# Optimization experiments

Hardware: AMD Instinct MI355X
Metric: run time of the kernel (lower is better)

## Reference

```python
import jax, jax.numpy as jnp
import numpy as np


def conv3x3(x, w, b):
    # stride 1, pad 1, NCHW / OIHW
    out = jax.lax.conv_general_dilated(x, w, (1, 1), ((1, 1), (1, 1)),
                                       dimension_numbers=('NCHW', 'OIHW', 'NCHW'))
    return out + b[None, :, None, None]


def bilinear_sample(x, ys, xs):
    # x: [B,C,H,W]; ys,xs: [B,K,H,W] float sampling coords.
    # mmcv-style: zero outside image, per-corner validity.
    B, C, H, W = x.shape
    x_flat = x.reshape(B, C, H * W)
    y0 = jnp.floor(ys)
    x0 = jnp.floor(xs)
    dy = ys - y0
    dx = xs - x0
    y0i = y0.astype(jnp.int32)
    x0i = x0.astype(jnp.int32)

    def corner(yc, xc, wgt):
        valid = (yc >= 0) & (yc < H) & (xc >= 0) & (xc < W)
        idx = jnp.clip(yc, 0, H - 1) * W + jnp.clip(xc, 0, W - 1)  # [B,K,H,W]
        idx_f = idx.reshape(B, -1)
        vals = jax.vmap(lambda xf, ix: xf[:, ix])(x_flat, idx_f)  # [B,C,K*H*W]
        vals = vals.reshape(B, C, *yc.shape[1:])
        return vals * (wgt * valid)[:, None]

    out = corner(y0i, x0i, (1 - dy) * (1 - dx))
    out = out + corner(y0i, x0i + 1, (1 - dy) * dx)
    out = out + corner(y0i + 1, x0i, dy * (1 - dx))
    out = out + corner(y0i + 1, x0i + 1, dy * dx)
    return out  # [B,C,K,H,W]


def avgpool3s2(z):
    # AvgPool2d(kernel=3, stride=2, padding=1), count_include_pad=True -> divide by 9
    s = jax.lax.reduce_window(z, 0.0, jax.lax.add, (1, 1, 3, 3), (1, 1, 2, 2),
                              ((0, 0), (0, 0), (1, 1), (1, 1)))
    return s / 9.0


def setup_inputs() -> dict:
    key = jax.random.key(0)
    k1, k2, k3 = jax.random.split(key, 3)
    C = 64
    x = jax.random.normal(k1, (4, C, 128, 128), dtype=jnp.float32)
    w_off = jax.random.normal(k2, (27, C, 3, 3), dtype=jnp.float32) * 0.02
    b_off = jnp.zeros((27,), dtype=jnp.float32)
    w_align = jax.random.normal(k3, (C, C, 3, 3), dtype=jnp.float32) * 0.02
    b_align = jnp.zeros((C,), dtype=jnp.float32)
    return {"x": x, "w_off": w_off, "b_off": b_off, "w_align": w_align, "b_align": b_align}


def reference(x, w_off, b_off, w_align, b_align):
    B, C, H, W = x.shape
    K = 9
    off_all = conv3x3(x, w_off, b_off)               # [B,27,H,W]
    offset = off_all[:, :2 * K]                      # [B,18,H,W]
    mask = 2.0 * jax.nn.sigmoid(off_all[:, 2 * K:])  # [B,9,H,W]
    off = offset.reshape(B, K, 2, H, W)
    dy = off[:, :, 0]
    dx = off[:, :, 1]
    # base kernel grid (dilation 1, pad 1): offsets in {-1,0,1}
    ky = (jnp.arange(K) // 3 - 1).astype(jnp.float32)
    kx = (jnp.arange(K) % 3 - 1).astype(jnp.float32)
    ys = jnp.arange(H, dtype=jnp.float32)[None, None, :, None] + ky[None, :, None, None] + dy
    xs = jnp.arange(W, dtype=jnp.float32)[None, None, None, :] + kx[None, :, None, None] + dx
    sampled = bilinear_sample(x, ys, xs) * mask[:, None]    # [B,C,K,H,W]
    w = jnp.einsum('bckhw,ock->bohw', sampled, w_align.reshape(C, C, K))
    w = w + b_align[None, :, None, None]
    w = jnp.exp(jax.nn.sigmoid(w))
    return avgpool3s2(w * x) / avgpool3s2(w)
```

## Files before the change

kernel.cpp:

```cpp
#include <hip/hip_runtime.h>
#include <hip/hip_bf16.h>

#define HW 16384
#define CC 64
#define BB 4

typedef __attribute__((ext_vector_type(8))) short bf8;
typedef __attribute__((ext_vector_type(4))) float f4;

static __device__ __forceinline__ unsigned short f2bf(float f) {
    __hip_bfloat16 h = __float2bfloat16(f);
    return *reinterpret_cast<unsigned short*>(&h);
}
static __device__ __forceinline__ float lo16f(unsigned u) { return __uint_as_float(u << 16); }
static __device__ __forceinline__ float hi16f(unsigned u) { return __uint_as_float(u & 0xFFFF0000u); }
static __device__ __forceinline__ unsigned rne_pack(float flo, float fhi) {
    unsigned a = __float_as_uint(flo);
    unsigned b = __float_as_uint(fhi);
    a += 0x7FFFu + ((a >> 16) & 1u);
    b += 0x7FFFu + ((b >> 16) & 1u);
    return __builtin_amdgcn_perm(b, a, 0x07060302u);
}

__global__ __launch_bounds__(256) void k_prep_tx(const float* __restrict__ x,
                                                 const float* __restrict__ w_off,
                                                 const float* __restrict__ w_align,
                                                 unsigned short* __restrict__ xT,
                                                 unsigned short* __restrict__ wA2,
                                                 unsigned short* __restrict__ Wal2) {
    __shared__ unsigned T32[64 * 33];
    int bx = blockIdx.x, t = threadIdx.x;
    if (bx < 216) {
        int i = bx * 256 + t;
        if (i < 32 * 576) {
            int jj = i & 7;
            int chunk = i >> 3;
            int l = chunk & 63;
            int g = chunk >> 6;
            int m2 = g & 1;
            int h2 = (g >> 1) & 1;
            int tp = g >> 2;
            int m = m2 * 16 + (l & 15);
            int c = h2 * 32 + (l >> 4) * 8 + jj;
            float v = (m < 27) ? w_off[m * 576 + c * 9 + tp] : 0.f;
            wA2[i] = f2bf(v);
        } else {
            int j = i - 32 * 576;
            int jj = j & 7;
            int chunk = j >> 3;
            int l = chunk & 63;
            int g = chunk >> 6;
            int mt = g & 3;
            int th = g >> 2;
            int h2 = th & 1;
            int tp = th >> 1;
            int o = mt * 16 + (l & 15);
            int c = h2 * 32 + (l >> 4) * 8 + jj;
            Wal2[j] = f2bf(w_align[o * 576 + c * 9 + tp]);
        }
        return;
    }
    int pix0 = (bx - 216) * 64;
    int b = pix0 >> 14, hw0 = pix0 & (HW - 1);
    const float* xb = x + (size_t)b * CC * HW + hw0;
#pragma unroll
    for (int u = 0; u < 8; u++) {
        int i = t + 256 * u;
        int cp = i >> 6, p = i & 63;
        float v0 = xb[(size_t)(2 * cp) * HW + p];
        float v1 = xb[(size_t)(2 * cp + 1) * HW + p];
        T32[p * 33 + cp] = (unsigned)f2bf(v0) | ((unsigned)f2bf(v1) << 16);
    }
    __syncthreads();
#pragma unroll
    for (int u = 0; u < 2; u++) {
        int i = t + 256 * u;
        int p = i >> 3, q = i & 7;
        uint4 qq;
        qq.x = T32[p * 33 + q * 4 + 0];
        qq.y = T32[p * 33 + q * 4 + 1];
        qq.z = T32[p * 33 + q * 4 + 2];
        qq.w = T32[p * 33 + q * 4 + 3];
        *(uint4*)(xT + ((size_t)b * HW + hw0 + p) * CC + q * 8) = qq;
    }
}

#define MIXD(P,M) rne_pack( \
    P##w0*lo16f(P##q0.M)+P##w1*lo16f(P##q1.M)+P##w2*lo16f(P##q2.M)+P##w3*lo16f(P##q3.M), \
    P##w0*hi16f(P##q0.M)+P##w1*hi16f(P##q1.M)+P##w2*hi16f(P##q2.M)+P##w3*hi16f(P##q3.M))
#define MIXD2(P,M) rne_pack( \
    P##w0*lo16f(P##q4.M)+P##w1*lo16f(P##q5.M)+P##w2*lo16f(P##q6.M)+P##w3*lo16f(P##q7.M), \
    P##w0*hi16f(P##q4.M)+P##w1*hi16f(P##q5.M)+P##w2*hi16f(P##q6.M)+P##w3*hi16f(P##q7.M))

#define PREP(j,P) { \
    float dy_ = OB[(2*(j))*133+pxo]; \
    float dx_ = OB[(2*(j)+1)*133+pxo]; \
    float m_  = OB[(18+(j))*133+pxo]; \
    const int k3_ = (j)/3, kx_ = (j)-3*k3_; \
    float ys_ = (float)(hp+k3_-1)+dy_, xs_ = (float)(wp+kx_-1)+dx_; \
    float y0f_ = floorf(ys_), x0f_ = floorf(xs_); \
    float fy_ = ys_-y0f_, fx_ = xs_-x0f_; \
    int y0_ = (int)y0f_, x0_ = (int)x0f_, y1_ = y0_+1, x1_ = x0_+1; \
    bool vy0_ = (unsigned)y0_<128u, vy1_ = (unsigned)y1_<128u; \
    bool vx0_ = (unsigned)x0_<128u, vx1_ = (unsigned)x1_<128u; \
    int cy0_ = min(max(y0_,0),127), cy1_ = min(max(y1_,0),127); \
    int cx0_ = min(max(x0_,0),127), cx1_ = min(max(x1_,0),127); \
    P##w0 = (1.f-fy_)*(1.f-fx_)*((vy0_&&vx0_)?m_:0.f); \
    P##w1 = (1.f-fy_)*fx_      *((vy0_&&vx1_)?m_:0.f); \
    P##w2 = fy_*(1.f-fx_)      *((vy1_&&vx0_)?m_:0.f); \
    P##w3 = fy_*fx_            *((vy1_&&vx1_)?m_:0.f); \
    bool inT_ = (cy0_>=hm2)&(cy1_<=hp3)&(cx0_>=wm3)&(cx1_<=wp66); \
    int r0_ = (cy0_-hm2)*70-wm3, r1_ = (cy1_-hm2)*70-wm3; \
    int e00_ = r0_+cx0_, e01_ = r0_+cx1_, e10_ = r1_+cx0_, e11_ = r1_+cx1_; \
    const unsigned short* p00_ = inT_ ? (TFg + e00_*64 + ((quad^(e00_&7))<<3)) \
        : xTb + ((size_t)((cy0_<<7)+cx0_))*CC + quad*8; \
    const unsigned short* p01_ = inT_ ? (TFg + e01_*64 + ((quad^(e01_&7))<<3)) \
        : xTb + ((size_t)((cy0_<<7)+cx1_))*CC + quad*8; \
    const unsigned short* p10_ = inT_ ? (TFg + e10_*64 + ((quad^(e10_&7))<<3)) \
        : xTb + ((size_t)((cy1_<<7)+cx0_))*CC + quad*8; \
    const unsigned short* p11_ = inT_ ? (TFg + e11_*64 + ((quad^(e11_&7))<<3)) \
        : xTb + ((size_t)((cy1_<<7)+cx1_))*CC + quad*8; \
    P##q0 = *(const uint4*)p00_; \
    P##q1 = *(const uint4*)p01_; \
    P##q2 = *(const uint4*)p10_; \
    P##q3 = *(const uint4*)p11_; \
    P##q4 = *(const uint4*)((unsigned long long)p00_ ^ 64ull); \
    P##q5 = *(const uint4*)((unsigned long long)p01_ ^ 64ull); \
    P##q6 = *(const uint4*)((unsigned long long)p10_ ^ 64ull); \
    P##q7 = *(const uint4*)((unsigned long long)p11_ ^ 64ull); \
}

#define TAP(j,P) { \
    uint4 f0_; \
    f0_.x = MIXD(P,x); f0_.y = MIXD(P,y); f0_.z = MIXD(P,z); f0_.w = MIXD(P,w); \
    uint4 f1_; \
    f1_.x = MIXD2(P,x); f1_.y = MIXD2(P,y); f1_.z = MIXD2(P,z); f1_.w = MIXD2(P,w); \
    bf8 bf0_ = *(const bf8*)&f0_; \
    bf8 bf1_ = *(const bf8*)&f1_; \
    const bf8 a0_ = *(const bf8*)(wl + (size_t)((((j)*2+0)*4+0)*512)); \
    const bf8 a1_ = *(const bf8*)(wl + (size_t)((((j)*2+0)*4+1)*512)); \
    const bf8 a2_ = *(const bf8*)(wl + (size_t)((((j)*2+0)*4+2)*512)); \
    const bf8 a3_ = *(const bf8*)(wl + (size_t)((((j)*2+0)*4+3)*512)); \
    acc[0] = __builtin_amdgcn_mfma_f32_16x16x32_bf16(a0_, bf0_, acc[0], 0, 0, 0); \
    acc[1] = __builtin_amdgcn_mfma_f32_16x16x32_bf16(a1_, bf0_, acc[1], 0, 0, 0); \
    acc[2] = __builtin_amdgcn_mfma_f32_16x16x32_bf16(a2_, bf0_, acc[2], 0, 0, 0); \
    acc[3] = __builtin_amdgcn_mfma_f32_16x16x32_bf16(a3_, bf0_, acc[3], 0, 0, 0); \
    const bf8 a4_ = *(const bf8*)(wl + (size_t)((((j)*2+1)*4+0)*512)); \
    const bf8 a5_ = *(const bf8*)(wl + (size_t)((((j)*2+1)*4+1)*512)); \
    const bf8 a6_ = *(const bf8*)(wl + (size_t)((((j)*2+1)*4+2)*512)); \
    const bf8 a7_ = *(const bf8*)(wl + (size_t)((((j)*2+1)*4+3)*512)); \
    acc[0] = __builtin_amdgcn_mfma_f32_16x16x32_bf16(a4_, bf1_, acc[0], 0, 0, 0); \
    acc[1] = __builtin_amdgcn_mfma_f32_16x16x32_bf16(a5_, bf1_, acc[1], 0, 0, 0); \
    acc[2] = __builtin_amdgcn_mfma_f32_16x16x32_bf16(a6_, bf1_, acc[2], 0, 0, 0); \
    acc[3] = __builtin_amdgcn_mfma_f32_16x16x32_bf16(a7_, bf1_, acc[3], 0, 0, 0); \
}

__global__ __launch_bounds__(512, 3) void k_fused(const unsigned short* __restrict__ xT,
                                                  const unsigned short* __restrict__ wA2,
                                                  const unsigned short* __restrict__ Wal2,
                                                  const float* __restrict__ b_off,
                                                  const float* __restrict__ b_align,
                                                  float* __restrict__ wten) {
    __shared__ __align__(16) unsigned short TF[420 * 64];
    __shared__ float OB[27 * 133];

    int t = threadIdx.x, lane = t & 63, wv = t >> 6;
    int quad = lane >> 4, col = lane & 15;
    int bx = blockIdx.x;
    int b = bx >> 7;
    int r = bx & 127;
    int h0 = (r >> 1) * 2;
    int w0 = (r & 1) * 64;
    int pxo = wv * 16 + col;
    int rr = pxo >> 6;
    int hp = h0 + rr, wp = w0 + (pxo & 63);
    int px = (hp << 7) + wp;
    const unsigned short* xTb = xT + (size_t)b * HW * CC;
    const unsigned short* wl = Wal2 + lane * 8;
    const unsigned short* TFg = TF;

#pragma unroll
    for (int u = 0; u < 7; u++) {
        int i = t + 512 * u;
        if (i < 3360) {
            int e = i >> 3, s = i & 7;
            int ty = e / 70, tx = e - ty * 70;
            int gy = min(max(h0 - 2 + ty, 0), 127);
            int gx = min(max(w0 - 3 + tx, 0), 127);
            int c = s ^ (e & 7);
            uint4 q = *(const uint4*)(xTb + ((size_t)((gy << 7) + gx)) * CC + c * 8);
            *(uint4*)(TF + i * 8) = q;
        }
    }
    __syncthreads();

    {
        const bf8 zero = {0, 0, 0, 0, 0, 0, 0, 0};
        f4 a0 = {0.f, 0.f, 0.f, 0.f};
        f4 a1 = {0.f, 0.f, 0.f, 0.f};
#pragma unroll
        for (int tap = 0; tap < 9; tap++) {
            int dyt = tap / 3 - 1, dxt = tap - (tap / 3) * 3 - 1;
            int hs = hp + dyt, ws = wp + dxt;
            bool valid = ((unsigned)hs < 128u) && ((unsigned)ws < 128u);
            int e = (rr + dyt + 2) * 70 + (pxo & 63) + dxt + 3;
            int sL = quad ^ (e & 7);
            bf8 b0 = *(const bf8*)(TF + e * 64 + (sL << 3));
            bf8 b1 = *(const bf8*)(TF + e * 64 + ((sL ^ 4) << 3));
            b0 = valid ? b0 : zero;
            b1 = valid ? b1 : zero;
            const bf8 a00 = *(const bf8*)(wA2 + (((tap * 4 + 0) * 64 + lane) << 3));
            const bf8 a01 = *(const bf8*)(wA2 + (((tap * 4 + 1) * 64 + lane) << 3));
            const bf8 a10 = *(const bf8*)(wA2 + (((tap * 4 + 2) * 64 + lane) << 3));
            const bf8 a11 = *(const bf8*)(wA2 + (((tap * 4 + 3) * 64 + lane) << 3));
            a0 = __builtin_amdgcn_mfma_f32_16x16x32_bf16(a00, b0, a0, 0, 0, 0);
            a1 = __builtin_amdgcn_mfma_f32_16x16x32_bf16(a01, b0, a1, 0, 0, 0);
            a0 = __builtin_amdgcn_mfma_f32_16x16x32_bf16(a10, b1, a0, 0, 0, 0);
            a1 = __builtin_amdgcn_mfma_f32_16x16x32_bf16(a11, b1, a1, 0, 0, 0);
        }
#pragma unroll
        for (int i = 0; i < 4; i++) {
            int o0 = quad * 4 + i;
            OB[o0 * 133 + pxo] = a0[i] + b_off[o0];
            int o1 = 16 + o0;
            if (o1 < 27) {
                float v = a1[i] + b_off[o1];
                if (o1 >= 18) v = 2.f / (1.f + __expf(-v));
                OB[o1 * 133 + pxo] = v;
            }
        }
    }

    int hm2 = h0 - 2, hp3 = h0 + 3, wm3 = w0 - 3, wp66 = w0 + 66;

    f4 acc[4];
#pragma unroll
    for (int mt = 0; mt < 4; mt++) acc[mt] = (f4){0.f, 0.f, 0.f, 0.f};

    uint4 Aq0, Aq1, Aq2, Aq3, Aq4, Aq5, Aq6, Aq7;
    uint4 Bq0, Bq1, Bq2, Bq3, Bq4, Bq5, Bq6, Bq7;
    float Aw0, Aw1, Aw2, Aw3, Bw0, Bw1, Bw2, Bw3;

    PREP(0, A);
    PREP(1, B); TAP(0, A);
    PREP(2, A); TAP(1, B);
    PREP(3, B); TAP(2, A);
    PREP(4, A); TAP(3, B);
    PREP(5, B); TAP(4, A);
    PREP(6, A); TAP(5, B);
    PREP(7, B); TAP(6, A);
    PREP(8, A); TAP(7, B);
    TAP(8, A);

    float* wb = wten + (size_t)b * CC * HW + px;
#pragma unroll
    for (int mt = 0; mt < 4; mt++)
#pragma unroll
        for (int i = 0; i < 4; i++) {
            int o = mt * 16 + quad * 4 + i;
            float u = acc[mt][i] + b_align[o];
            float sg = 1.f / (1.f + __expf(-u));
            wb[(size_t)o * HW] = __expf(sg);
        }
}

__global__ __launch_bounds__(256) void k_pool(const float* __restrict__ x,
                                              const float* __restrict__ wten,
                                              float* __restrict__ out) {
    int idx = blockIdx.x * 256 + threadIdx.x;
    int ow = idx & 63;
    int oh = (idx >> 6) & 63;
    int bc = idx >> 12;
    const float* wp = wten + (size_t)bc * HW;
    const float* xp = x + (size_t)bc * HW;
    float num = 0.f, den = 0.f;
#pragma unroll
    for (int iy = 0; iy < 3; iy++) {
        int y = 2 * oh + iy - 1;
        if ((unsigned)y >= 128u) continue;
#pragma unroll
        for (int ix = 0; ix < 3; ix++) {
            int xc = 2 * ow + ix - 1;
            if ((unsigned)xc >= 128u) continue;
            float wv = wp[y * 128 + xc];
            float xv = xp[y * 128 + xc];
            num = fmaf(wv, xv, num);
            den += wv;
        }
    }
    out[idx] = num / den;
}

extern "C" void kernel_launch(void* const* d_in, const int* in_sizes, int n_in,
                              void* d_out, int out_size, void* d_ws, size_t ws_size,
                              hipStream_t stream) {
    const float* x       = (const float*)d_in[0];
    const float* w_off   = (const float*)d_in[1];
    const float* b_off   = (const float*)d_in[2];
    const float* w_align = (const float*)d_in[3];
    const float* b_align = (const float*)d_in[4];
    float* out = (float*)d_out;

    char* p = (char*)d_ws;
    float* wten = (float*)p;                  p += (size_t)BB * CC * HW * 4;
    unsigned short* xT  = (unsigned short*)p; p += (size_t)BB * HW * CC * 2;
    unsigned short* wA2 = (unsigned short*)p; p += 32 * 576 * 2;
    unsigned short* Wal2 = (unsigned short*)p;

    k_prep_tx<<<dim3(1240), dim3(256), 0, stream>>>(x, w_off, w_align, xT, wA2, Wal2);
    k_fused<<<dim3(512), dim3(512), 0, stream>>>(xT, wA2, Wal2, b_off, b_align, wten);
    k_pool<<<dim3(4096), dim3(256), 0, stream>>>(x, wten, out);
}
```

Before: 117.3 us.

## Apply bilinear weights after MFMA instead of mixing corner samples before

Instead of blending the four bilinear corner samples in fp32 and repacking them to bf16 before each MFMA, each corner's raw bf16 values are multiplied by the weights through MFMA separately. The corner weights are then applied to the per-corner results with FMAs into the accumulator. This removes the unpack, mix and RNE-repack ALU work but issues four times as many MFMAs per tap. Launch bounds also go from 3 to 4 blocks per CU, which tightens the register budget.

```diff
diff --git a/kernel.cpp b/kernel.cpp
--- a/kernel.cpp
+++ b/kernel.cpp
@@ -11,15 +11,6 @@
 static __device__ __forceinline__ unsigned short f2bf(float f) {
     __hip_bfloat16 h = __float2bfloat16(f);
     return *reinterpret_cast<unsigned short*>(&h);
-}
-static __device__ __forceinline__ float lo16f(unsigned u) { return __uint_as_float(u << 16); }
-static __device__ __forceinline__ float hi16f(unsigned u) { return __uint_as_float(u & 0xFFFF0000u); }
-static __device__ __forceinline__ unsigned rne_pack(float flo, float fhi) {
-    unsigned a = __float_as_uint(flo);
-    unsigned b = __float_as_uint(fhi);
-    a += 0x7FFFu + ((a >> 16) & 1u);
-    b += 0x7FFFu + ((b >> 16) & 1u);
-    return __builtin_amdgcn_perm(b, a, 0x07060302u);
 }
 
 __global__ __launch_bounds__(256) void k_prep_tx(const float* __restrict__ x,
@@ -84,13 +75,6 @@
         *(uint4*)(xT + ((size_t)b * HW + hw0 + p) * CC + q * 8) = qq;
     }
 }
-
-#define MIXD(P,M) rne_pack( \
-    P##w0*lo16f(P##q0.M)+P##w1*lo16f(P##q1.M)+P##w2*lo16f(P##q2.M)+P##w3*lo16f(P##q3.M), \
-    P##w0*hi16f(P##q0.M)+P##w1*hi16f(P##q1.M)+P##w2*hi16f(P##q2.M)+P##w3*hi16f(P##q3.M))
-#define MIXD2(P,M) rne_pack( \
-    P##w0*lo16f(P##q4.M)+P##w1*lo16f(P##q5.M)+P##w2*lo16f(P##q6.M)+P##w3*lo16f(P##q7.M), \
-    P##w0*hi16f(P##q4.M)+P##w1*hi16f(P##q5.M)+P##w2*hi16f(P##q6.M)+P##w3*hi16f(P##q7.M))
 
 #define PREP(j,P) { \
     float dy_ = OB[(2*(j))*133+pxo]; \
@@ -130,32 +114,31 @@
     P##q7 = *(const uint4*)((unsigned long long)p11_ ^ 64ull); \
 }
 
-#define TAP(j,P) { \
-    uint4 f0_; \
-    f0_.x = MIXD(P,x); f0_.y = MIXD(P,y); f0_.z = MIXD(P,z); f0_.w = MIXD(P,w); \
-    uint4 f1_; \
-    f1_.x = MIXD2(P,x); f1_.y = MIXD2(P,y); f1_.z = MIXD2(P,z); f1_.w = MIXD2(P,w); \
-    bf8 bf0_ = *(const bf8*)&f0_; \
-    bf8 bf1_ = *(const bf8*)&f1_; \
-    const bf8 a0_ = *(const bf8*)(wl + (size_t)((((j)*2+0)*4+0)*512)); \
-    const bf8 a1_ = *(const bf8*)(wl + (size_t)((((j)*2+0)*4+1)*512)); \
-    const bf8 a2_ = *(const bf8*)(wl + (size_t)((((j)*2+0)*4+2)*512)); \
-    const bf8 a3_ = *(const bf8*)(wl + (size_t)((((j)*2+0)*4+3)*512)); \
-    acc[0] = __builtin_amdgcn_mfma_f32_16x16x32_bf16(a0_, bf0_, acc[0], 0, 0, 0); \
-    acc[1] = __builtin_amdgcn_mfma_f32_16x16x32_bf16(a1_, bf0_, acc[1], 0, 0, 0); \
-    acc[2] = __builtin_amdgcn_mfma_f32_16x16x32_bf16(a2_, bf0_, acc[2], 0, 0, 0); \
-    acc[3] = __builtin_amdgcn_mfma_f32_16x16x32_bf16(a3_, bf0_, acc[3], 0, 0, 0); \
-    const bf8 a4_ = *(const bf8*)(wl + (size_t)((((j)*2+1)*4+0)*512)); \
-    const bf8 a5_ = *(const bf8*)(wl + (size_t)((((j)*2+1)*4+1)*512)); \
-    const bf8 a6_ = *(const bf8*)(wl + (size_t)((((j)*2+1)*4+2)*512)); \
-    const bf8 a7_ = *(const bf8*)(wl + (size_t)((((j)*2+1)*4+3)*512)); \
-    acc[0] = __builtin_amdgcn_mfma_f32_16x16x32_bf16(a4_, bf1_, acc[0], 0, 0, 0); \
-    acc[1] = __builtin_amdgcn_mfma_f32_16x16x32_bf16(a5_, bf1_, acc[1], 0, 0, 0); \
-    acc[2] = __builtin_amdgcn_mfma_f32_16x16x32_bf16(a6_, bf1_, acc[2], 0, 0, 0); \
-    acc[3] = __builtin_amdgcn_mfma_f32_16x16x32_bf16(a7_, bf1_, acc[3], 0, 0, 0); \
-}
-
-__global__ __launch_bounds__(512, 3) void k_fused(const unsigned short* __restrict__ xT,
+#define TAP1(j,P,MT) { \
+    const bf8 ah0_ = *(const bf8*)(wl + (size_t)((((j)*2+0)*4+(MT))*512)); \
+    const bf8 ah1_ = *(const bf8*)(wl + (size_t)((((j)*2+1)*4+(MT))*512)); \
+    const f4 z_ = {0.f, 0.f, 0.f, 0.f}; \
+    f4 t0_ = __builtin_amdgcn_mfma_f32_16x16x32_bf16(ah0_, *(const bf8*)&P##q0, z_, 0, 0, 0); \
+    t0_    = __builtin_amdgcn_mfma_f32_16x16x32_bf16(ah1_, *(const bf8*)&P##q4, t0_, 0, 0, 0); \
+    f4 t1_ = __builtin_amdgcn_mfma_f32_16x16x32_bf16(ah0_, *(const bf8*)&P##q1, z_, 0, 0, 0); \
+    t1_    = __builtin_amdgcn_mfma_f32_16x16x32_bf16(ah1_, *(const bf8*)&P##q5, t1_, 0, 0, 0); \
+    f4 t2_ = __builtin_amdgcn_mfma_f32_16x16x32_bf16(ah0_, *(const bf8*)&P##q2, z_, 0, 0, 0); \
+    t2_    = __builtin_amdgcn_mfma_f32_16x16x32_bf16(ah1_, *(const bf8*)&P##q6, t2_, 0, 0, 0); \
+    f4 t3_ = __builtin_amdgcn_mfma_f32_16x16x32_bf16(ah0_, *(const bf8*)&P##q3, z_, 0, 0, 0); \
+    t3_    = __builtin_amdgcn_mfma_f32_16x16x32_bf16(ah1_, *(const bf8*)&P##q7, t3_, 0, 0, 0); \
+    _Pragma("unroll") \
+    for (int i_ = 0; i_ < 4; i_++) { \
+        float s_ = acc[MT][i_]; \
+        s_ = fmaf(P##w0, t0_[i_], s_); \
+        s_ = fmaf(P##w1, t1_[i_], s_); \
+        s_ = fmaf(P##w2, t2_[i_], s_); \
+        s_ = fmaf(P##w3, t3_[i_], s_); \
+        acc[MT][i_] = s_; \
+    } \
+}
+#define TAP(j,P) { TAP1(j,P,0) TAP1(j,P,1) TAP1(j,P,2) TAP1(j,P,3) }
+
+__global__ __launch_bounds__(512, 4) void k_fused(const unsigned short* __restrict__ xT,
                                                   const unsigned short* __restrict__ wA2,
                                                   const unsigned short* __restrict__ Wal2,
                                                   const float* __restrict__ b_off,
```

New measurement: 370.5 us. 216% more time.
